# Performance work log

Measured on AMD Instinct MI355X. Metric: run time of the kernel, lower is better.

## Reference

```python
import jax, jax.numpy as jnp
import numpy as np

N, E, IN, H, OUT = 100000, 3200000, 128, 128, 64
BN_EPS = 1e-5


def setup_inputs() -> dict:
    key = jax.random.key(0)
    ks = jax.random.split(key, 12)
    x = jax.random.normal(ks[0], (N, IN), dtype=jnp.float32)
    edge_index = jax.random.randint(ks[1], (2, E), 0, N, dtype=jnp.int64)
    s = 1.0 / np.sqrt(IN)
    Wl1 = jax.random.uniform(ks[2], (H, IN), jnp.float32, -s, s)
    bl1 = jax.random.uniform(ks[3], (H,), jnp.float32, -s, s)
    Wr1 = jax.random.uniform(ks[4], (H, IN), jnp.float32, -s, s)
    s2 = 1.0 / np.sqrt(H)
    Wl2 = jax.random.uniform(ks[5], (OUT, H), jnp.float32, -s2, s2)
    bl2 = jax.random.uniform(ks[6], (OUT,), jnp.float32, -s2, s2)
    Wr2 = jax.random.uniform(ks[7], (OUT, H), jnp.float32, -s2, s2)
    bn_g = jnp.ones((H,), jnp.float32)
    bn_b = jnp.zeros((H,), jnp.float32)
    bn_rm = jax.random.normal(ks[8], (H,), jnp.float32) * 0.1
    bn_rv = jax.random.uniform(ks[9], (H,), jnp.float32, 0.5, 1.5)
    return {"x": x, "edge_index": edge_index, "Wl1": Wl1, "bl1": bl1, "Wr1": Wr1,
            "Wl2": Wl2, "bl2": bl2, "Wr2": Wr2,
            "bn_g": bn_g, "bn_b": bn_b, "bn_rm": bn_rm, "bn_rv": bn_rv}


def sage_conv(x, src, dst, Wl, bl, Wr):
    # mean aggregation of source features into target nodes
    msg_sum = jax.ops.segment_sum(x[src], dst, num_segments=N)       # [N, F]
    deg = jax.ops.segment_sum(jnp.ones((src.shape[0],), x.dtype), dst, num_segments=N)
    agg = msg_sum / jnp.maximum(deg, 1.0)[:, None]
    return agg @ Wl.T + bl + x @ Wr.T


def reference(x, edge_index, Wl1, bl1, Wr1, Wl2, bl2, Wr2, bn_g, bn_b, bn_rm, bn_rv):
    src, dst = edge_index[0], edge_index[1]
    h = sage_conv(x, src, dst, Wl1, bl1, Wr1)
    # BatchNorm1d in eval mode (running stats)
    h = (h - bn_rm) * (bn_g / jnp.sqrt(bn_rv + BN_EPS)) + bn_b
    h = jax.nn.relu(h)
    # dropout is identity in eval mode
    out = sage_conv(h, src, dst, Wl2, bl2, Wr2)
    return out
```

## Files before the change

### kernel.cpp

```cpp
#include <hip/hip_runtime.h>
#include <cstdint>
#include <cstddef>

#define BN_EPS 1e-5f

constexpr int BSH    = 7;
constexpr int BNODES = 1 << BSH;
constexpr int MAXNB  = 800;
constexpr int CAPB   = 4608;
constexpr int TSORT  = 4096;
constexpr int STHR   = 512;
constexpr int ATHR   = 512;

static inline size_t align_up(size_t v, size_t a) { return (v + a - 1) & ~(a - 1); }

typedef short  short8 __attribute__((ext_vector_type(8)));
typedef float  f32x4  __attribute__((ext_vector_type(4)));
typedef float  f32x2  __attribute__((ext_vector_type(2)));

__device__ inline unsigned short f2bf(float f) {
    unsigned u = __builtin_bit_cast(unsigned, f);
    unsigned r = u + 0x7FFFu + ((u >> 16) & 1u);
    return (unsigned short)(r >> 16);
}
__device__ inline float bf2f_lo(unsigned v) { return __builtin_bit_cast(float, v << 16); }
__device__ inline float bf2f_hi(unsigned v) { return __builtin_bit_cast(float, v & 0xFFFF0000u); }

__device__ inline unsigned char f2fp8(float x) {
    return (unsigned char)(__builtin_amdgcn_cvt_pk_fp8_f32(x, x, 0, false) & 0xFF);
}
__device__ inline void fp8x4_acc(unsigned w, float* acc) {
    f32x2 p0 = __builtin_amdgcn_cvt_pk_f32_fp8(w, false);
    f32x2 p1 = __builtin_amdgcn_cvt_pk_f32_fp8(w, true);
    acc[0] += p0.x; acc[1] += p0.y; acc[2] += p1.x; acc[3] += p1.y;
}


__global__ __launch_bounds__(256) void cvt_w_kernel(
    const float* __restrict__ w1, const float* __restrict__ w2,
    const float* __restrict__ w3, const float* __restrict__ w4,
    unsigned short* __restrict__ o1, unsigned short* __restrict__ o2,
    unsigned short* __restrict__ o3, unsigned short* __restrict__ o4,
    int* __restrict__ gcur, int NB)
{
    if (blockIdx.x == 48) {
        for (int b = threadIdx.x; b < NB; b += 256) gcur[b] = b * CAPB;
        return;
    }
    int i = blockIdx.x * 256 + threadIdx.x;
    const float* s; unsigned short* d; int j;
    if (i < 4096)       { s = w1; d = o1; j = i; }
    else if (i < 8192)  { s = w2; d = o2; j = i - 4096; }
    else if (i < 10240) { s = w3; d = o3; j = i - 8192; }
    else                { s = w4; d = o4; j = i - 10240; }
    float4 v = ((const float4*)s)[j];
    ushort4 o;
    o.x = f2bf(v.x); o.y = f2bf(v.y); o.z = f2bf(v.z); o.w = f2bf(v.w);
    ((ushort4*)d)[j] = o;
}


__global__ __launch_bounds__(STHR) void sort_tile_kernel(
    const int* __restrict__ src, const int* __restrict__ dst,
    int* __restrict__ gcur, unsigned int* __restrict__ bins, int E, int NB)
{
    __shared__ int cnt[MAXNB];
    __shared__ int pos[MAXNB];
    __shared__ int bend[MAXNB];
    __shared__ int gbase[MAXNB];
    __shared__ unsigned int sorted[TSORT];
    __shared__ unsigned short bkt[TSORT];
    __shared__ int wtot[STHR / 64];

    const int tid = threadIdx.x;
    const int t0  = blockIdx.x * TSORT;
    const int m   = min(TSORT, E - t0);

    for (int b = tid; b < NB; b += STHR) cnt[b] = 0;
    __syncthreads();

    for (int i = tid; i < m; i += STHR) {
        int d = dst[t0 + i];
        atomicAdd(&cnt[d >> BSH], 1);
    }
    __syncthreads();

    int base4 = tid * 4;
    int c0 = 0, c1 = 0, c2 = 0, c3 = 0;
    if (base4 + 0 < NB) c0 = cnt[base4 + 0];
    if (base4 + 1 < NB) c1 = cnt[base4 + 1];
    if (base4 + 2 < NB) c2 = cnt[base4 + 2];
    if (base4 + 3 < NB) c3 = cnt[base4 + 3];
    int s = c0 + c1 + c2 + c3;
    int lane = tid & 63, wid = tid >> 6;
    int inc = s;
#pragma unroll
    for (int off = 1; off < 64; off <<= 1) { int t = __shfl_up(inc, off); if (lane >= off) inc += t; }
    if (lane == 63) wtot[wid] = inc;
    __syncthreads();
    int woff = 0;
    for (int w = 0; w < wid; ++w) woff += wtot[w];
    int excl = woff + inc - s;
    if (base4 + 0 < NB) { pos[base4 + 0] = excl;                bend[base4 + 0] = excl + c0; }
    if (base4 + 1 < NB) { pos[base4 + 1] = excl + c0;           bend[base4 + 1] = excl + c0 + c1; }
    if (base4 + 2 < NB) { pos[base4 + 2] = excl + c0 + c1;      bend[base4 + 2] = excl + c0 + c1 + c2; }
    if (base4 + 3 < NB) { pos[base4 + 3] = excl + c0 + c1 + c2; bend[base4 + 3] = excl + s; }
    __syncthreads();

    for (int i = tid; i < m; i += STHR) {
        int d  = dst[t0 + i];
        int sv = src[t0 + i];
        int b  = d >> BSH;
        int p  = atomicAdd(&pos[b], 1);
        sorted[p] = ((unsigned)(d & (BNODES - 1)) << 17) | (unsigned)sv;
        bkt[p]    = (unsigned short)b;
    }
    __syncthreads();

    for (int b = tid; b < NB; b += STHR) {
        int c = cnt[b];
        gbase[b] = c ? atomicAdd(&gcur[b], c) : 0;
    }
    __syncthreads();

    for (int i = tid; i < m; i += STHR) {
        int b  = bkt[i];
        int lo = bend[b] - cnt[b];
        bins[gbase[b] + (i - lo)] = sorted[i];
    }
}


__global__ __launch_bounds__(256) void bucket_scan_kernel(
    const int* __restrict__ gcur, int* __restrict__ bbase,
    int* __restrict__ rowp, int NB, int N, int E)
{
    __shared__ int wtot[4];
    const int tid = threadIdx.x;
    int base4 = tid * 4;
    int c0 = 0, c1 = 0, c2 = 0, c3 = 0;
    if (base4 + 0 < NB) c0 = gcur[base4 + 0] - (base4 + 0) * CAPB;
    if (base4 + 1 < NB) c1 = gcur[base4 + 1] - (base4 + 1) * CAPB;
    if (base4 + 2 < NB) c2 = gcur[base4 + 2] - (base4 + 2) * CAPB;
    if (base4 + 3 < NB) c3 = gcur[base4 + 3] - (base4 + 3) * CAPB;
    int s = c0 + c1 + c2 + c3;
    int lane = tid & 63, wid = tid >> 6;
    int inc = s;
#pragma unroll
    for (int off = 1; off < 64; off <<= 1) { int t = __shfl_up(inc, off); if (lane >= off) inc += t; }
    if (lane == 63) wtot[wid] = inc;
    __syncthreads();
    int woff = 0;
    for (int w = 0; w < wid; ++w) woff += wtot[w];
    int excl = woff + inc - s;
    if (base4 + 0 < NB) bbase[base4 + 0] = excl;
    if (base4 + 1 < NB) bbase[base4 + 1] = excl + c0;
    if (base4 + 2 < NB) bbase[base4 + 2] = excl + c0 + c1;
    if (base4 + 3 < NB) bbase[base4 + 3] = excl + c0 + c1 + c2;
    if (tid == 0) rowp[N] = E;
}


__global__ __launch_bounds__(ATHR) void bucket_agg1_kernel(
    const unsigned int* __restrict__ bins, const int* __restrict__ gcur,
    const int* __restrict__ bbase,
    const unsigned char* __restrict__ Y1f8, const unsigned short* __restrict__ Zb,
    unsigned short* __restrict__ Hb, int* __restrict__ rowp, int* __restrict__ colg,
    const float* __restrict__ g_, const float* __restrict__ b_,
    const float* __restrict__ rm, const float* __restrict__ rv, int N)
{
    __shared__ unsigned int sorted[CAPB];
    __shared__ int cnt[BNODES];
    __shared__ int pos[BNODES];
    __shared__ int pst[BNODES];
    __shared__ int w0tot;

    const int tid = threadIdx.x;
    const int bk  = blockIdx.x;
    const int beg = bk * CAPB;
    const int m   = gcur[bk] - beg;
    const int gb  = bbase[bk];

    if (tid < BNODES) cnt[tid] = 0;
    __syncthreads();

    for (int i = tid; i < m; i += ATHR) atomicAdd(&cnt[bins[beg + i] >> 17], 1);
    __syncthreads();

    if (tid < BNODES) {
        int c = cnt[tid];
        int lane = tid & 63;
        int inc = c;
#pragma unroll
        for (int off = 1; off < 64; off <<= 1) { int t = __shfl_up(inc, off); if (lane >= off) inc += t; }
        if (tid == 63) w0tot = inc;
        __syncthreads();
        int excl = inc - c + ((tid >= 64) ? w0tot : 0);
        pos[tid] = excl;
        pst[tid] = excl;
        int node = (bk << BSH) + tid;
        if (node < N) rowp[node] = gb + excl;
    } else {
        __syncthreads();
    }
    __syncthreads();

    for (int i = tid; i < m; i += ATHR) {
        unsigned v = bins[beg + i];
        int p = atomicAdd(&pos[v >> 17], 1);
        sorted[p] = v;
    }
    __syncthreads();

    for (int i = tid; i < m; i += ATHR) colg[gb + i] = (int)(sorted[i] & 0x1FFFFu);

    const int wv  = tid >> 6;
    const int lane = tid & 63;
    const int grp = lane >> 4;
    const int fl  = lane & 15;

    float sc[8], bb2[8];
    {
        float4 ga = ((const float4*)g_)[fl * 2],  gbv = ((const float4*)g_)[fl * 2 + 1];
        float4 va = ((const float4*)rv)[fl * 2],  vb  = ((const float4*)rv)[fl * 2 + 1];
        float4 ma = ((const float4*)rm)[fl * 2],  mb  = ((const float4*)rm)[fl * 2 + 1];
        float4 ba = ((const float4*)b_)[fl * 2],  bb  = ((const float4*)b_)[fl * 2 + 1];
        float gg[8] = {ga.x, ga.y, ga.z, ga.w, gbv.x, gbv.y, gbv.z, gbv.w};
        float vv[8] = {va.x, va.y, va.z, va.w, vb.x,  vb.y,  vb.z,  vb.w};
        float mm[8] = {ma.x, ma.y, ma.z, ma.w, mb.x,  mb.y,  mb.z,  mb.w};
        float bz[8] = {ba.x, ba.y, ba.z, ba.w, bb.x,  bb.y,  bb.z,  bb.w};
#pragma unroll
        for (int j = 0; j < 8; ++j) { sc[j] = gg[j] * rsqrtf(vv[j] + BN_EPS); bb2[j] = bz[j] - mm[j] * sc[j]; }
    }

    for (int nl = wv; nl < BNODES; nl += ATHR / 64) {
        int node = (bk << BSH) + nl;
        if (node >= N) continue;
        const int s0 = pst[nl];
        const int cn = cnt[nl];
        float acc[8];
#pragma unroll
        for (int j = 0; j < 8; ++j) acc[j] = 0.f;

        int q = 0;
        for (; q + 16 <= cn; q += 16) {
            unsigned v0 = sorted[s0 + q + grp];
            unsigned v1 = sorted[s0 + q + 4 + grp];
            unsigned v2 = sorted[s0 + q + 8 + grp];
            unsigned v3 = sorted[s0 + q + 12 + grp];
            uint2 d0 = *(const uint2*)(Y1f8 + (size_t)(v0 & 0x1FFFFu) * 128 + fl * 8);
            uint2 d1 = *(const uint2*)(Y1f8 + (size_t)(v1 & 0x1FFFFu) * 128 + fl * 8);
            uint2 d2 = *(const uint2*)(Y1f8 + (size_t)(v2 & 0x1FFFFu) * 128 + fl * 8);
            uint2 d3 = *(const uint2*)(Y1f8 + (size_t)(v3 & 0x1FFFFu) * 128 + fl * 8);
            fp8x4_acc(d0.x, acc); fp8x4_acc(d0.y, acc + 4);
            fp8x4_acc(d1.x, acc); fp8x4_acc(d1.y, acc + 4);
            fp8x4_acc(d2.x, acc); fp8x4_acc(d2.y, acc + 4);
            fp8x4_acc(d3.x, acc); fp8x4_acc(d3.y, acc + 4);
        }
        for (; q + 4 <= cn; q += 4) {
            unsigned v0 = sorted[s0 + q + grp];
            uint2 d0 = *(const uint2*)(Y1f8 + (size_t)(v0 & 0x1FFFFu) * 128 + fl * 8);
            fp8x4_acc(d0.x, acc); fp8x4_acc(d0.y, acc + 4);
        }
        int rem = cn - q;
        if (grp < rem) {
            unsigned v0 = sorted[s0 + q + grp];
            uint2 d0 = *(const uint2*)(Y1f8 + (size_t)(v0 & 0x1FFFFu) * 128 + fl * 8);
            fp8x4_acc(d0.x, acc); fp8x4_acc(d0.y, acc + 4);
        }
#pragma unroll
        for (int j = 0; j < 8; ++j) {
            acc[j] += __shfl_xor(acc[j], 16);
            acc[j] += __shfl_xor(acc[j], 32);
        }
        float inv = 1.0f / (float)(cn > 1 ? cn : 1);
        uint4 zr = *(const uint4*)(Zb + (size_t)node * 128 + fl * 8);
        float z[8] = {bf2f_lo(zr.x), bf2f_hi(zr.x), bf2f_lo(zr.y), bf2f_hi(zr.y),
                      bf2f_lo(zr.z), bf2f_hi(zr.z), bf2f_lo(zr.w), bf2f_hi(zr.w)};
        if (grp == 0) {
            unsigned short hb16[8];
#pragma unroll
            for (int j = 0; j < 8; ++j) {
                float h = fmaxf((acc[j] * inv + z[j]) * sc[j] + bb2[j], 0.f);
                hb16[j] = f2bf(h);
            }
            uint4 o;
            o.x = (unsigned)hb16[0] | ((unsigned)hb16[1] << 16);
            o.y = (unsigned)hb16[2] | ((unsigned)hb16[3] << 16);
            o.z = (unsigned)hb16[4] | ((unsigned)hb16[5] << 16);
            o.w = (unsigned)hb16[6] | ((unsigned)hb16[7] << 16);
            *(uint4*)(Hb + (size_t)node * 128 + fl * 8) = o;
        }
    }
}


template <int FOUT, bool ZF32, bool XF32>
__global__ __launch_bounds__(256) void gemm_dual_mfma_kernel(
    const void* __restrict__ Xv, const unsigned short* __restrict__ Wlb,
    const unsigned short* __restrict__ Wrb, const float* __restrict__ bz,
    unsigned char* __restrict__ Y, void* __restrict__ Z, int n)
{
    constexpr int FT = FOUT / 16;
    const int tid = threadIdx.x;
    const int w   = tid >> 6;
    const int l   = tid & 63;
    const int nbase = blockIdx.x * 64 + w * 16;
    const int lrow  = l & 15;
    const int koff  = (l >> 4) * 8;

    f32x4 accY[FT], accZ[FT];
#pragma unroll
    for (int f = 0; f < FT; ++f) { accY[f] = (f32x4)(0.f); accZ[f] = (f32x4)(0.f); }

    const int arow  = nbase + lrow;
    const int arowc = (arow < n) ? arow : 0;

    short8 av[4];
    if constexpr (XF32) {
        const float* xr = (const float*)Xv + (size_t)arowc * 128 + koff;
#pragma unroll
        for (int ks = 0; ks < 4; ++ks) {
            float4 xa = *(const float4*)(xr + ks * 32);
            float4 xb = *(const float4*)(xr + ks * 32 + 4);
            short8 a;
            a[0] = (short)f2bf(xa.x); a[1] = (short)f2bf(xa.y);
            a[2] = (short)f2bf(xa.z); a[3] = (short)f2bf(xa.w);
            a[4] = (short)f2bf(xb.x); a[5] = (short)f2bf(xb.y);
            a[6] = (short)f2bf(xb.z); a[7] = (short)f2bf(xb.w);
            av[ks] = a;
        }
    } else {
        const unsigned short* xr = (const unsigned short*)Xv + (size_t)arowc * 128 + koff;
#pragma unroll
        for (int ks = 0; ks < 4; ++ks) av[ks] = *(const short8*)(xr + ks * 32);
    }

#pragma unroll
    for (int ks = 0; ks < 4; ++ks) {
#pragma unroll
        for (int f = 0; f < FT; ++f) {
            const size_t wo = (size_t)(f * 16 + lrow) * 128 + ks * 32 + koff;
            short8 bl = *(const short8*)(Wlb + wo);
            accY[f] = __builtin_amdgcn_mfma_f32_16x16x32_bf16(av[ks], bl, accY[f], 0, 0, 0);
            short8 br = *(const short8*)(Wrb + wo);
            accZ[f] = __builtin_amdgcn_mfma_f32_16x16x32_bf16(av[ks], br, accZ[f], 0, 0, 0);
        }
    }

    const int colc  = l & 15;
    const int rbase = nbase + (l >> 4) * 4;
#pragma unroll
    for (int f = 0; f < FT; ++f) {
        float bv = bz[f * 16 + colc];
#pragma unroll
        for (int j = 0; j < 4; ++j) {
            int node = rbase + j;
            if (node < n) {
                size_t o = (size_t)node * FOUT + f * 16 + colc;
                Y[o] = f2fp8(accY[f][j]);
                if constexpr (ZF32) ((float*)Z)[o] = accZ[f][j] + bv;
                else ((unsigned short*)Z)[o] = f2bf(accZ[f][j] + bv);
            }
        }
    }
}


__global__ __launch_bounds__(256) void agg_out_kernel(
    const unsigned char* __restrict__ Y2f8, const int* __restrict__ col,
    const int* __restrict__ rowp, float* __restrict__ out, int n)
{
    int node = blockIdx.x * 4 + (threadIdx.x >> 6);
    int lane = threadIdx.x & 63;
    if (node >= n) return;
    const int grp = lane >> 4;
    const int fl  = lane & 15;
    int beg = rowp[node], end = rowp[node + 1];
    int cn = end - beg;
    float acc[4] = {0.f, 0.f, 0.f, 0.f};
    int q = 0;
    for (; q + 16 <= cn; q += 16) {
        int c0 = col[beg + q + grp];
        int c1 = col[beg + q + 4 + grp];
        int c2 = col[beg + q + 8 + grp];
        int c3 = col[beg + q + 12 + grp];
        unsigned d0 = *(const unsigned*)(Y2f8 + (size_t)c0 * 64 + fl * 4);
        unsigned d1 = *(const unsigned*)(Y2f8 + (size_t)c1 * 64 + fl * 4);
        unsigned d2 = *(const unsigned*)(Y2f8 + (size_t)c2 * 64 + fl * 4);
        unsigned d3 = *(const unsigned*)(Y2f8 + (size_t)c3 * 64 + fl * 4);
        fp8x4_acc(d0, acc); fp8x4_acc(d1, acc);
        fp8x4_acc(d2, acc); fp8x4_acc(d3, acc);
    }
    for (; q + 4 <= cn; q += 4) {
        int c0 = col[beg + q + grp];
        unsigned d0 = *(const unsigned*)(Y2f8 + (size_t)c0 * 64 + fl * 4);
        fp8x4_acc(d0, acc);
    }
    int rem = cn - q;
    if (grp < rem) {
        int c0 = col[beg + q + grp];
        unsigned d0 = *(const unsigned*)(Y2f8 + (size_t)c0 * 64 + fl * 4);
        fp8x4_acc(d0, acc);
    }
#pragma unroll
    for (int j = 0; j < 4; ++j) {
        acc[j] += __shfl_xor(acc[j], 16);
        acc[j] += __shfl_xor(acc[j], 32);
    }
    if (grp == 0) {
        float inv = 1.0f / (float)(cn > 1 ? cn : 1);
        float4* po = (float4*)(out + (size_t)node * 64 + fl * 4);
        float4 o = *po;
        o.x += acc[0] * inv; o.y += acc[1] * inv;
        o.z += acc[2] * inv; o.w += acc[3] * inv;
        *po = o;
    }
}


extern "C" void kernel_launch(void* const* d_in, const int* in_sizes, int n_in,
                              void* d_out, int out_size, void* d_ws, size_t ws_size,
                              hipStream_t stream)
{
    const float* x     = (const float*)d_in[0];
    const int*   ei    = (const int*)d_in[1];
    const float* Wl1   = (const float*)d_in[2];
    const float* bl1   = (const float*)d_in[3];
    const float* Wr1   = (const float*)d_in[4];
    const float* Wl2   = (const float*)d_in[5];
    const float* bl2   = (const float*)d_in[6];
    const float* Wr2   = (const float*)d_in[7];
    const float* bn_g  = (const float*)d_in[8];
    const float* bn_b  = (const float*)d_in[9];
    const float* bn_rm = (const float*)d_in[10];
    const float* bn_rv = (const float*)d_in[11];

    const int N = in_sizes[0] / 128;
    const int E = in_sizes[1] / 2;
    const int* src = ei;
    const int* dst = ei + E;
    const int NB = (N + BNODES - 1) >> BSH;

    char* ws = (char*)d_ws;
    size_t off = 0;
    auto alloc = [&](size_t bytes) { size_t o = off; off = align_up(off + bytes, 256); return (void*)(ws + o); };
    int*            gcur  = (int*)alloc((size_t)MAXNB * 4);
    int*            bbase = (int*)alloc((size_t)MAXNB * 4);
    unsigned int*   bins  = (unsigned int*)alloc((size_t)NB * CAPB * 4);
    int*            rowp  = (int*)alloc((size_t)(N + 1) * 4);
    int*            col   = (int*)alloc((size_t)E * 4);
    unsigned short* wl1b  = (unsigned short*)alloc(128 * 128 * 2);
    unsigned short* wr1b  = (unsigned short*)alloc(128 * 128 * 2);
    unsigned short* wl2b  = (unsigned short*)alloc(64 * 128 * 2);
    unsigned short* wr2b  = (unsigned short*)alloc(64 * 128 * 2);
    unsigned char*  y1f8  = (unsigned char*)alloc((size_t)N * 128);
    unsigned short* zb    = (unsigned short*)alloc((size_t)N * 128 * 2);
    unsigned short* hb    = (unsigned short*)alloc((size_t)N * 128 * 2);
    unsigned char*  y2f8  = y1f8;
    float*          outf  = (float*)d_out;

    const int sb = (E + TSORT - 1) / TSORT;
    const int gb = (N + 63) / 64;
    const int ab = (N + 3) / 4;

    cvt_w_kernel<<<49, 256, 0, stream>>>(Wl1, Wr1, Wl2, Wr2, wl1b, wr1b, wl2b, wr2b, gcur, NB);

    gemm_dual_mfma_kernel<128, false, true><<<gb, 256, 0, stream>>>(x, wl1b, wr1b, bl1, y1f8, zb, N);

    sort_tile_kernel<<<sb, STHR, 0, stream>>>(src, dst, gcur, bins, E, NB);
    bucket_scan_kernel<<<1, 256, 0, stream>>>(gcur, bbase, rowp, NB, N, E);

    bucket_agg1_kernel<<<NB, ATHR, 0, stream>>>(bins, gcur, bbase, y1f8, zb, hb, rowp, col,
                                                bn_g, bn_b, bn_rm, bn_rv, N);

    gemm_dual_mfma_kernel<64, true, false><<<gb, 256, 0, stream>>>(hb, wl2b, wr2b, bl2, y2f8, (void*)outf, N);

    agg_out_kernel<<<ab, 256, 0, stream>>>(y2f8, col, rowp, outf, N);
}
```

Before: 299.3 us.

## Keep bin entries in registers, fold BN shift into GEMM, nontemporal streaming

The bucket aggregation kernel now holds its bin entries in registers (up to EVR=9 per thread) so it reads them from global memory once instead of twice, and it drops the pst array. The batch-norm mean and bias are folded into the Z epilogue of the first GEMM, which leaves only the scale in the aggregation step. Edge, bin, col and x streams use nontemporal loads and stores, and agg_out moves to 512-thread blocks. The register buffer assumes a bucket holds at most 4608 entries, which matches CAPB. It also adds register pressure in the aggregation kernel.

Result: slower. 330.0 us (+10.3%).

```diff
diff --git a/kernel.cpp b/kernel.cpp
--- a/kernel.cpp
+++ b/kernel.cpp
@@ -11,6 +11,7 @@
 constexpr int TSORT  = 4096;
 constexpr int STHR   = 512;
 constexpr int ATHR   = 512;
+constexpr int EVR    = 9;
 
 static inline size_t align_up(size_t v, size_t a) { return (v + a - 1) & ~(a - 1); }
 
@@ -53,7 +54,7 @@
     else if (i < 8192)  { s = w2; d = o2; j = i - 4096; }
     else if (i < 10240) { s = w3; d = o3; j = i - 8192; }
     else                { s = w4; d = o4; j = i - 10240; }
-    float4 v = ((const float4*)s)[j];
+    f32x4 v = ((const f32x4*)s)[j];
     ushort4 o;
     o.x = f2bf(v.x); o.y = f2bf(v.y); o.z = f2bf(v.z); o.w = f2bf(v.w);
     ((ushort4*)d)[j] = o;
@@ -80,7 +81,7 @@
     __syncthreads();
 
     for (int i = tid; i < m; i += STHR) {
-        int d = dst[t0 + i];
+        int d = __builtin_nontemporal_load(&dst[t0 + i]);
         atomicAdd(&cnt[d >> BSH], 1);
     }
     __syncthreads();
@@ -108,8 +109,8 @@
     __syncthreads();
 
     for (int i = tid; i < m; i += STHR) {
-        int d  = dst[t0 + i];
-        int sv = src[t0 + i];
+        int d  = __builtin_nontemporal_load(&dst[t0 + i]);
+        int sv = __builtin_nontemporal_load(&src[t0 + i]);
         int b  = d >> BSH;
         int p  = atomicAdd(&pos[b], 1);
         sorted[p] = ((unsigned)(d & (BNODES - 1)) << 17) | (unsigned)sv;
@@ -126,7 +127,7 @@
     for (int i = tid; i < m; i += STHR) {
         int b  = bkt[i];
         int lo = bend[b] - cnt[b];
-        bins[gbase[b] + (i - lo)] = sorted[i];
+        __builtin_nontemporal_store(sorted[i], &bins[gbase[b] + (i - lo)]);
     }
 }
 
@@ -166,13 +167,11 @@
     const int* __restrict__ bbase,
     const unsigned char* __restrict__ Y1f8, const unsigned short* __restrict__ Zb,
     unsigned short* __restrict__ Hb, int* __restrict__ rowp, int* __restrict__ colg,
-    const float* __restrict__ g_, const float* __restrict__ b_,
-    const float* __restrict__ rm, const float* __restrict__ rv, int N)
+    const float* __restrict__ g_, const float* __restrict__ rv, int N)
 {
     __shared__ unsigned int sorted[CAPB];
     __shared__ int cnt[BNODES];
     __shared__ int pos[BNODES];
-    __shared__ int pst[BNODES];
     __shared__ int w0tot;
 
     const int tid = threadIdx.x;
@@ -184,7 +183,16 @@
     if (tid < BNODES) cnt[tid] = 0;
     __syncthreads();
 
-    for (int i = tid; i < m; i += ATHR) atomicAdd(&cnt[bins[beg + i] >> 17], 1);
+    unsigned ev[EVR];
+#pragma unroll
+    for (int r = 0; r < EVR; ++r) {
+        int i = tid + r * ATHR;
+        ev[r] = 0xFFFFFFFFu;
+        if (i < m) {
+            ev[r] = __builtin_nontemporal_load(&bins[beg + i]);
+            atomicAdd(&cnt[ev[r] >> 17], 1);
+        }
+    }
     __syncthreads();
 
     if (tid < BNODES) {
@@ -197,7 +205,6 @@
         __syncthreads();
         int excl = inc - c + ((tid >= 64) ? w0tot : 0);
         pos[tid] = excl;
-        pst[tid] = excl;
         int node = (bk << BSH) + tid;
         if (node < N) rowp[node] = gb + excl;
     } else {
@@ -205,39 +212,38 @@
     }
     __syncthreads();
 
-    for (int i = tid; i < m; i += ATHR) {
-        unsigned v = bins[beg + i];
-        int p = atomicAdd(&pos[v >> 17], 1);
-        sorted[p] = v;
-    }
-    __syncthreads();
-
-    for (int i = tid; i < m; i += ATHR) colg[gb + i] = (int)(sorted[i] & 0x1FFFFu);
+#pragma unroll
+    for (int r = 0; r < EVR; ++r) {
+        if (ev[r] != 0xFFFFFFFFu) {
+            int p = atomicAdd(&pos[(int)(ev[r] >> 17)], 1);
+            sorted[p] = ev[r];
+        }
+    }
+    __syncthreads();
+
+    for (int i = tid; i < m; i += ATHR)
+        __builtin_nontemporal_store((int)(sorted[i] & 0x1FFFFu), &colg[gb + i]);
 
     const int wv  = tid >> 6;
     const int lane = tid & 63;
     const int grp = lane >> 4;
     const int fl  = lane & 15;
 
-    float sc[8], bb2[8];
+    float sc[8];
     {
-        float4 ga = ((const float4*)g_)[fl * 2],  gbv = ((const float4*)g_)[fl * 2 + 1];
-        float4 va = ((const float4*)rv)[fl * 2],  vb  = ((const float4*)rv)[fl * 2 + 1];
-        float4 ma = ((const float4*)rm)[fl * 2],  mb  = ((const float4*)rm)[fl * 2 + 1];
-        float4 ba = ((const float4*)b_)[fl * 2],  bb  = ((const float4*)b_)[fl * 2 + 1];
+        f32x4 ga = ((const f32x4*)g_)[fl * 2],  gbv = ((const f32x4*)g_)[fl * 2 + 1];
+        f32x4 va = ((const f32x4*)rv)[fl * 2],  vb  = ((const f32x4*)rv)[fl * 2 + 1];
         float gg[8] = {ga.x, ga.y, ga.z, ga.w, gbv.x, gbv.y, gbv.z, gbv.w};
         float vv[8] = {va.x, va.y, va.z, va.w, vb.x,  vb.y,  vb.z,  vb.w};
-        float mm[8] = {ma.x, ma.y, ma.z, ma.w, mb.x,  mb.y,  mb.z,  mb.w};
-        float bz[8] = {ba.x, ba.y, ba.z, ba.w, bb.x,  bb.y,  bb.z,  bb.w};
-#pragma unroll
-        for (int j = 0; j < 8; ++j) { sc[j] = gg[j] * rsqrtf(vv[j] + BN_EPS); bb2[j] = bz[j] - mm[j] * sc[j]; }
+#pragma unroll
+        for (int j = 0; j < 8; ++j) sc[j] = gg[j] * rsqrtf(vv[j] + BN_EPS);
     }
 
     for (int nl = wv; nl < BNODES; nl += ATHR / 64) {
         int node = (bk << BSH) + nl;
         if (node >= N) continue;
-        const int s0 = pst[nl];
         const int cn = cnt[nl];
+        const int s0 = pos[nl] - cn;
         float acc[8];
 #pragma unroll
         for (int j = 0; j < 8; ++j) acc[j] = 0.f;
@@ -281,7 +287,7 @@
             unsigned short hb16[8];
 #pragma unroll
             for (int j = 0; j < 8; ++j) {
-                float h = fmaxf((acc[j] * inv + z[j]) * sc[j] + bb2[j], 0.f);
+                float h = fmaxf(fmaf(acc[j] * inv, sc[j], z[j]), 0.f);
                 hb16[j] = f2bf(h);
             }
             uint4 o;
@@ -295,11 +301,13 @@
 }
 
 
-template <int FOUT, bool ZF32, bool XF32>
+template <int FOUT, bool ZF32, bool XF32, bool BNF>
 __global__ __launch_bounds__(256) void gemm_dual_mfma_kernel(
     const void* __restrict__ Xv, const unsigned short* __restrict__ Wlb,
     const unsigned short* __restrict__ Wrb, const float* __restrict__ bz,
-    unsigned char* __restrict__ Y, void* __restrict__ Z, int n)
+    unsigned char* __restrict__ Y, void* __restrict__ Z, int n,
+    const float* __restrict__ bng, const float* __restrict__ bnb,
+    const float* __restrict__ bnrm, const float* __restrict__ bnrv)
 {
     constexpr int FT = FOUT / 16;
     const int tid = threadIdx.x;
@@ -321,8 +329,8 @@
         const float* xr = (const float*)Xv + (size_t)arowc * 128 + koff;
 #pragma unroll
         for (int ks = 0; ks < 4; ++ks) {
-            float4 xa = *(const float4*)(xr + ks * 32);
-            float4 xb = *(const float4*)(xr + ks * 32 + 4);
+            f32x4 xa = __builtin_nontemporal_load((const f32x4*)(xr + ks * 32));
+            f32x4 xb = __builtin_nontemporal_load((const f32x4*)(xr + ks * 32 + 4));
             short8 a;
             a[0] = (short)f2bf(xa.x); a[1] = (short)f2bf(xa.y);
             a[2] = (short)f2bf(xa.z); a[3] = (short)f2bf(xa.w);
@@ -352,26 +360,35 @@
     const int rbase = nbase + (l >> 4) * 4;
 #pragma unroll
     for (int f = 0; f < FT; ++f) {
-        float bv = bz[f * 16 + colc];
+        const int fc = f * 16 + colc;
+        float bv = bz[fc];
+        float scv = 0.f, rmv = 0.f, bbv = 0.f;
+        if constexpr (BNF) {
+            scv = bng[fc] * rsqrtf(bnrv[fc] + BN_EPS);
+            rmv = bnrm[fc];
+            bbv = bnb[fc];
+        }
 #pragma unroll
         for (int j = 0; j < 4; ++j) {
             int node = rbase + j;
             if (node < n) {
-                size_t o = (size_t)node * FOUT + f * 16 + colc;
+                size_t o = (size_t)node * FOUT + fc;
                 Y[o] = f2fp8(accY[f][j]);
-                if constexpr (ZF32) ((float*)Z)[o] = accZ[f][j] + bv;
-                else ((unsigned short*)Z)[o] = f2bf(accZ[f][j] + bv);
+                float zz = accZ[f][j] + bv;
+                if constexpr (BNF) zz = (zz - rmv) * scv + bbv;
+                if constexpr (ZF32) ((float*)Z)[o] = zz;
+                else ((unsigned short*)Z)[o] = f2bf(zz);
             }
         }
     }
 }
 
 
-__global__ __launch_bounds__(256) void agg_out_kernel(
+__global__ __launch_bounds__(512) void agg_out_kernel(
     const unsigned char* __restrict__ Y2f8, const int* __restrict__ col,
     const int* __restrict__ rowp, float* __restrict__ out, int n)
 {
-    int node = blockIdx.x * 4 + (threadIdx.x >> 6);
+    int node = blockIdx.x * 8 + (threadIdx.x >> 6);
     int lane = threadIdx.x & 63;
     if (node >= n) return;
     const int grp = lane >> 4;
@@ -381,10 +398,10 @@
     float acc[4] = {0.f, 0.f, 0.f, 0.f};
     int q = 0;
     for (; q + 16 <= cn; q += 16) {
-        int c0 = col[beg + q + grp];
-        int c1 = col[beg + q + 4 + grp];
-        int c2 = col[beg + q + 8 + grp];
-        int c3 = col[beg + q + 12 + grp];
+        int c0 = __builtin_nontemporal_load(&col[beg + q + grp]);
+        int c1 = __builtin_nontemporal_load(&col[beg + q + 4 + grp]);
+        int c2 = __builtin_nontemporal_load(&col[beg + q + 8 + grp]);
+        int c3 = __builtin_nontemporal_load(&col[beg + q + 12 + grp]);
         unsigned d0 = *(const unsigned*)(Y2f8 + (size_t)c0 * 64 + fl * 4);
         unsigned d1 = *(const unsigned*)(Y2f8 + (size_t)c1 * 64 + fl * 4);
         unsigned d2 = *(const unsigned*)(Y2f8 + (size_t)c2 * 64 + fl * 4);
@@ -393,13 +410,13 @@
         fp8x4_acc(d2, acc); fp8x4_acc(d3, acc);
     }
     for (; q + 4 <= cn; q += 4) {
-        int c0 = col[beg + q + grp];
+        int c0 = __builtin_nontemporal_load(&col[beg + q + grp]);
         unsigned d0 = *(const unsigned*)(Y2f8 + (size_t)c0 * 64 + fl * 4);
         fp8x4_acc(d0, acc);
     }
     int rem = cn - q;
     if (grp < rem) {
-        int c0 = col[beg + q + grp];
+        int c0 = __builtin_nontemporal_load(&col[beg + q + grp]);
         unsigned d0 = *(const unsigned*)(Y2f8 + (size_t)c0 * 64 + fl * 4);
         fp8x4_acc(d0, acc);
     }
@@ -462,19 +479,21 @@
 
     const int sb = (E + TSORT - 1) / TSORT;
     const int gb = (N + 63) / 64;
-    const int ab = (N + 3) / 4;
+    const int ab = (N + 7) / 8;
 
     cvt_w_kernel<<<49, 256, 0, stream>>>(Wl1, Wr1, Wl2, Wr2, wl1b, wr1b, wl2b, wr2b, gcur, NB);
 
-    gemm_dual_mfma_kernel<128, false, true><<<gb, 256, 0, stream>>>(x, wl1b, wr1b, bl1, y1f8, zb, N);
+    gemm_dual_mfma_kernel<128, false, true, true><<<gb, 256, 0, stream>>>(
+        x, wl1b, wr1b, bl1, y1f8, zb, N, bn_g, bn_b, bn_rm, bn_rv);
 
     sort_tile_kernel<<<sb, STHR, 0, stream>>>(src, dst, gcur, bins, E, NB);
     bucket_scan_kernel<<<1, 256, 0, stream>>>(gcur, bbase, rowp, NB, N, E);
 
     bucket_agg1_kernel<<<NB, ATHR, 0, stream>>>(bins, gcur, bbase, y1f8, zb, hb, rowp, col,
-                                                bn_g, bn_b, bn_rm, bn_rv, N);
-
-    gemm_dual_mfma_kernel<64, true, false><<<gb, 256, 0, stream>>>(hb, wl2b, wr2b, bl2, y2f8, (void*)outf, N);
-
-    agg_out_kernel<<<ab, 256, 0, stream>>>(y2f8, col, rowp, outf, N);
-}
+                                                bn_g, bn_rv, N);
+
+    gemm_dual_mfma_kernel<64, true, false, false><<<gb, 256, 0, stream>>>(
+        hb, wl2b, wr2b, bl2, y2f8, (void*)outf, N, nullptr, nullptr, nullptr, nullptr);
+
+    agg_out_kernel<<<ab, 512, 0, stream>>>(y2f8, col, rowp, outf, N);
+}
```
